# Optimization experiments

Hardware: AMD Instinct MI355X
Metric: run time of the kernel (lower is better)

The kernel has to match this reference:

```python
import jax, jax.numpy as jnp
import numpy as np

IN_DIM = 128
HID = 128
OUT = 128

def _linear(x, W, b):
    return x @ W + b

def setup_inputs() -> dict:
    key = jax.random.key(0)
    ks = jax.random.split(key, 16)
    B, N = 2, 512
    def w(k, fan_in, fan_out):
        lim = 1.0 / np.sqrt(fan_in)
        return jax.random.uniform(k, (fan_in, fan_out), jnp.float32, -lim, lim)
    def bvec(k, fan_in, fan_out):
        lim = 1.0 / np.sqrt(fan_in)
        return jax.random.uniform(k, (fan_out,), jnp.float32, -lim, lim)
    return {
        "features": jax.random.normal(ks[0], (B, N, IN_DIM), jnp.float32),
        "coords": jax.random.normal(ks[1], (B, N, 3), jnp.float32),
        "eW1": w(ks[2], 2 * IN_DIM + 1, HID), "eb1": bvec(ks[3], 2 * IN_DIM + 1, HID),
        "eW2": w(ks[4], HID, HID), "eb2": bvec(ks[5], HID, HID),
        "nW1": w(ks[6], IN_DIM + HID, HID), "nb1": bvec(ks[7], IN_DIM + HID, HID),
        "nW2": w(ks[8], HID, OUT), "nb2": bvec(ks[9], HID, OUT),
        "cW1": w(ks[10], HID, HID), "cb1": bvec(ks[11], HID, HID),
        "cW2": w(ks[12], HID, 1), "cb2": bvec(ks[13], HID, 1),
    }

def reference(features, coords, eW1, eb1, eW2, eb2, nW1, nb1, nW2, nb2, cW1, cb1, cW2, cb2):
    B, N, D = features.shape
    # pairwise coordinate differences and distances: (B, N, N, 3), (B, N, N, 1)
    coord_diff = coords[:, :, None, :] - coords[:, None, :, :]
    distances = jnp.sqrt(jnp.sum(coord_diff ** 2, axis=-1, keepdims=True) + 1e-8)
    # all-pairs edge features: (B, N, N, 2D+1)
    feat_i = jnp.broadcast_to(features[:, :, None, :], (B, N, N, D))
    feat_j = jnp.broadcast_to(features[:, None, :, :], (B, N, N, D))
    edge_features = jnp.concatenate([feat_i, feat_j, distances], axis=-1)
    edge_hidden = _linear(jax.nn.silu(_linear(edge_features, eW1, eb1)), eW2, eb2)
    # mean over neighbors j -> (B, N, HID)
    aggregated = jnp.mean(edge_hidden, axis=2)
    node_input = jnp.concatenate([features, aggregated], axis=-1)
    updated_features = _linear(jax.nn.silu(_linear(node_input, nW1, nb1)), nW2, nb2)
    # coordinate update
    coord_weights = _linear(jax.nn.silu(_linear(edge_hidden, cW1, cb1)), cW2, cb2)  # (B,N,N,1)
    updated_coords = coords + jnp.mean(coord_weights * coord_diff, axis=2)
    return (updated_features, updated_coords)
```

## Files before the change

kernel.cpp:

```cpp
#include <hip/hip_runtime.h>
#include <hip/hip_bf16.h>
#include <math.h>


typedef float f32x4 __attribute__((ext_vector_type(4)));
typedef short short8 __attribute__((ext_vector_type(8)));

#define MFMA16(a, b, c) __builtin_amdgcn_mfma_f32_16x16x32_bf16((a), (b), (c), 0, 0, 0)

__device__ __forceinline__ short f2bf(float x) {
    __hip_bfloat16 h = __float2bfloat16(x);
    union { __hip_bfloat16 h; short s; } v; v.h = h;
    return v.s;
}
__device__ __forceinline__ float bf2f(short s) {
    union { unsigned u; float f; } v; v.u = ((unsigned)(unsigned short)s) << 16;
    return v.f;
}
__device__ __forceinline__ float silu_f(float x) {
    return x * __builtin_amdgcn_rcpf(1.0f + __expf(-x));
}

__device__ __forceinline__ int swz(int row, int col) {
    int byte = (row << 8) | (col << 1);
    byte ^= (row & 7) << 4;
    return byte >> 1;
}

__global__ void egnn_pre(const float* __restrict__ feat, const float* __restrict__ eW1,
                         const float* __restrict__ eb1,
                         float* __restrict__ Abuf, float* __restrict__ Bbuf) {
    __shared__ float f[128];
    const int nid = blockIdx.x;
    const int t = threadIdx.x;
    if (t < 128) f[t] = feat[nid * 128 + t];
    __syncthreads();
    const int col  = t & 127;
    const int half = t >> 7;
    const float* W = eW1 + (size_t)half * 128 * 128 + col;
    float acc = half ? 0.f : eb1[col];
    #pragma unroll 8
    for (int k = 0; k < 128; ++k) acc += f[k] * W[(size_t)k * 128];
    if (half == 0) Abuf[nid * 128 + col] = acc;
    else           Bbuf[nid * 128 + col] = acc;
}

__global__ void egnn_wprep(const float* __restrict__ eW2, const float* __restrict__ cW1,
                           const float* __restrict__ eb2, const float* __restrict__ cb1,
                           unsigned short* __restrict__ MbfT, float* __restrict__ bias2ws) {
    const int a = blockIdx.x;
    const int c = threadIdx.x;
    if (a < 128) {
        float acc = 0.f;
        #pragma unroll 8
        for (int h = 0; h < 128; ++h) acc += eW2[a * 128 + h] * cW1[h * 128 + c];
        MbfT[c * 128 + a] = (unsigned short)f2bf(acc);
    } else {
        float acc = cb1[c];
        #pragma unroll 8
        for (int h = 0; h < 128; ++h) acc += eb2[h] * cW1[h * 128 + c];
        bias2ws[c] = acc;
    }
}

__global__ void __launch_bounds__(256, 2) egnn_main(
    const float* __restrict__ coords, const float* __restrict__ eW1,
    const float* __restrict__ cW2, const float* __restrict__ cb2,
    const float* __restrict__ Abuf, const float* __restrict__ Bbuf,
    const unsigned short* __restrict__ MbfT, const float* __restrict__ bias2ws,
    float* __restrict__ aggpart, float* __restrict__ coordpart)
{
    constexpr int Nn = 512;
    __shared__ __align__(16) short se[64 * 128];
    __shared__ float aw[128], wd[128];
    __shared__ float cdp[2][3][64];
    __shared__ float warr[2][4][64];
    __shared__ float aggred[16][128];
    __shared__ float cred[4][3];
    __shared__ float ci3[3];

    const int tid  = threadIdx.x;
    const int lane = tid & 63;
    const int wave = tid >> 6;
    const int bid  = blockIdx.x;
    const int node = bid >> 1;
    const int half = bid & 1;
    const int b    = node >> 9;

    if (tid < 128) {
        aw[tid] = Abuf[node * 128 + tid];
        wd[tid] = eW1[256 * 128 + tid];
    }
    if (tid == 0) {
        ci3[0] = coords[node * 3 + 0];
        ci3[1] = coords[node * 3 + 1];
        ci3[2] = coords[node * 3 + 2];
    }

    const int cfrag = wave * 32 + (lane & 15);
    const int koff  = (lane >> 4) * 8;
    short8 wfM[2][4];
    #pragma unroll
    for (int n2 = 0; n2 < 2; ++n2)
        #pragma unroll
        for (int k = 0; k < 4; ++k)
            wfM[n2][k] = *(const short8*)&MbfT[(size_t)(cfrag + n2 * 16) * 128 + k * 32 + koff];
    __syncthreads();

    const float b2_0  = bias2ws[cfrag], b2_1 = bias2ws[cfrag + 16];
    const float cw2_0 = cW2[cfrag],     cw2_1 = cW2[cfrag + 16];
    const float cb2v  = cb2[0];
    const float cix = ci3[0], ciy = ci3[1], ciz = ci3[2];

    const int jr = tid >> 2, cb = (tid & 3) * 32;
    const int rg = tid >> 4, c8 = (tid & 15) * 8;

    float ap[8];
    #pragma unroll
    for (int q = 0; q < 8; ++q) ap[q] = 0.f;
    float cax = 0.f, cay = 0.f, caz = 0.f;

    for (int t = 0; t < 4; ++t) {
        const int par = t & 1;
        {
            const int j = half * 256 + t * 64 + jr;
            const float dx = cix - coords[(b * Nn + j) * 3 + 0];
            const float dy = ciy - coords[(b * Nn + j) * 3 + 1];
            const float dz = ciz - coords[(b * Nn + j) * 3 + 2];
            const float dj = sqrtf(dx * dx + dy * dy + dz * dz + 1e-8f);
            if ((tid & 3) == 0) {
                cdp[par][0][jr] = dx; cdp[par][1][jr] = dy; cdp[par][2][jr] = dz;
            }
            const float* Bj = Bbuf + (size_t)(b * Nn + j) * 128 + cb;
            #pragma unroll
            for (int cc = 0; cc < 32; cc += 8) {
                f32x4 x0 = *(const f32x4*)(Bj + cc);
                f32x4 x1 = *(const f32x4*)(Bj + cc + 4);
                short8 v;
                #pragma unroll
                for (int r = 0; r < 4; ++r) {
                    const int c = cb + cc + r;
                    v[r] = f2bf(silu_f(aw[c] + x0[r] + dj * wd[c]));
                }
                #pragma unroll
                for (int r = 0; r < 4; ++r) {
                    const int c = cb + cc + 4 + r;
                    v[4 + r] = f2bf(silu_f(aw[c] + x1[r] + dj * wd[c]));
                }
                *(short8*)&se[swz(jr, cb + cc)] = v;
            }
        }
        __syncthreads();

        f32x4 acc[4][2];
        #pragma unroll
        for (int m = 0; m < 4; ++m) {
            acc[m][0] = (f32x4){b2_0, b2_0, b2_0, b2_0};
            acc[m][1] = (f32x4){b2_1, b2_1, b2_1, b2_1};
        }
        #pragma unroll
        for (int m = 0; m < 4; ++m)
            #pragma unroll
            for (int k = 0; k < 4; ++k) {
                short8 a = *(const short8*)&se[swz(m * 16 + (lane & 15), k * 32 + koff)];
                acc[m][0] = MFMA16(a, wfM[0][k], acc[m][0]);
                acc[m][1] = MFMA16(a, wfM[1][k], acc[m][1]);
            }

        #pragma unroll
        for (int r = 0; r < 4; ++r) {
            short8 v = *(const short8*)&se[swz(rg * 4 + r, c8)];
            #pragma unroll
            for (int q = 0; q < 8; ++q) ap[q] += bf2f(v[q]);
        }

        #pragma unroll
        for (int m = 0; m < 4; ++m)
            #pragma unroll
            for (int reg = 0; reg < 4; ++reg) {
                float v = silu_f(acc[m][0][reg]) * cw2_0
                        + silu_f(acc[m][1][reg]) * cw2_1;
                v += __shfl_xor(v, 1); v += __shfl_xor(v, 2);
                v += __shfl_xor(v, 4); v += __shfl_xor(v, 8);
                if ((lane & 15) == 0)
                    warr[par][wave][m * 16 + (lane >> 4) * 4 + reg] = v;
            }
        __syncthreads();

        if (lane < 16) {
            const int row = wave * 16 + lane;
            const float w = warr[par][0][row] + warr[par][1][row]
                          + warr[par][2][row] + warr[par][3][row] + cb2v;
            cax += w * cdp[par][0][row];
            cay += w * cdp[par][1][row];
            caz += w * cdp[par][2][row];
        }
    }

    #pragma unroll
    for (int q = 0; q < 8; ++q) aggred[rg][c8 + q] = ap[q];
    {
        float sx = cax, sy = cay, sz = caz;
        sx += __shfl_xor(sx, 1); sy += __shfl_xor(sy, 1); sz += __shfl_xor(sz, 1);
        sx += __shfl_xor(sx, 2); sy += __shfl_xor(sy, 2); sz += __shfl_xor(sz, 2);
        sx += __shfl_xor(sx, 4); sy += __shfl_xor(sy, 4); sz += __shfl_xor(sz, 4);
        sx += __shfl_xor(sx, 8); sy += __shfl_xor(sy, 8); sz += __shfl_xor(sz, 8);
        if (lane == 0) { cred[wave][0] = sx; cred[wave][1] = sy; cred[wave][2] = sz; }
    }
    __syncthreads();
    if (tid < 128) {
        float s = 0.f;
        #pragma unroll
        for (int g = 0; g < 16; ++g) s += aggred[g][tid];
        aggpart[(size_t)bid * 128 + tid] = s;
    }
    if (tid < 3) {
        coordpart[bid * 3 + tid] = cred[0][tid] + cred[1][tid] + cred[2][tid] + cred[3][tid];
    }
}

__global__ void egnn_post(
    const float* __restrict__ features, const float* __restrict__ coords,
    const float* __restrict__ eW2, const float* __restrict__ eb2,
    const float* __restrict__ nW1, const float* __restrict__ nb1,
    const float* __restrict__ nW2, const float* __restrict__ nb2,
    const float* __restrict__ aggpart, const float* __restrict__ coordpart,
    float* __restrict__ out_feat, float* __restrict__ out_coord)
{
    __shared__ float aggs[128], aggh[128], hbuf[128], fi[128];
    const int node = blockIdx.x;
    const int tid  = threadIdx.x;

    aggs[tid] = aggpart[(size_t)(node * 2) * 128 + tid]
              + aggpart[(size_t)(node * 2 + 1) * 128 + tid];
    fi[tid]   = features[node * 128 + tid];
    __syncthreads();
    {
        float acc = 0.f;
        #pragma unroll 4
        for (int c = 0; c < 128; ++c) acc += aggs[c] * eW2[c * 128 + tid];
        aggh[tid] = acc * (1.f / 512.f) + eb2[tid];
    }
    if (tid < 3) {
        out_coord[node * 3 + tid] = coords[node * 3 + tid]
            + (coordpart[(node * 2) * 3 + tid] + coordpart[(node * 2 + 1) * 3 + tid])
              * (1.f / 512.f);
    }
    __syncthreads();
    {
        float acc = nb1[tid];
        #pragma unroll 4
        for (int k = 0; k < 128; ++k) acc += fi[k] * nW1[k * 128 + tid];
        #pragma unroll 4
        for (int k = 0; k < 128; ++k) acc += aggh[k] * nW1[(128 + k) * 128 + tid];
        hbuf[tid] = silu_f(acc);
    }
    __syncthreads();
    {
        float acc = nb2[tid];
        #pragma unroll 4
        for (int k = 0; k < 128; ++k) acc += hbuf[k] * nW2[k * 128 + tid];
        out_feat[node * 128 + tid] = acc;
    }
}

extern "C" void kernel_launch(void* const* d_in, const int* in_sizes, int n_in,
                              void* d_out, int out_size, void* d_ws, size_t ws_size,
                              hipStream_t stream)
{
    const float* features = (const float*)d_in[0];
    const float* coords   = (const float*)d_in[1];
    const float* eW1 = (const float*)d_in[2];
    const float* eb1 = (const float*)d_in[3];
    const float* eW2 = (const float*)d_in[4];
    const float* eb2 = (const float*)d_in[5];
    const float* nW1 = (const float*)d_in[6];
    const float* nb1 = (const float*)d_in[7];
    const float* nW2 = (const float*)d_in[8];
    const float* nb2 = (const float*)d_in[9];
    const float* cW1 = (const float*)d_in[10];
    const float* cb1 = (const float*)d_in[11];
    const float* cW2 = (const float*)d_in[12];
    const float* cb2 = (const float*)d_in[13];

    float* out = (float*)d_out;
    float* out_feat  = out;
    float* out_coord = out + 2 * 512 * 128;

    float* Abuf      = (float*)d_ws;
    float* Bbuf      = Abuf + 2 * 512 * 128;
    unsigned short* MbfT = (unsigned short*)(Bbuf + 2 * 512 * 128);
    float* bias2ws   = (float*)(MbfT + 128 * 128);
    float* aggpart   = bias2ws + 128;
    float* coordpart = aggpart + 2048 * 128;

    egnn_pre<<<1024, 256, 0, stream>>>(features, eW1, eb1, Abuf, Bbuf);
    egnn_wprep<<<129, 128, 0, stream>>>(eW2, cW1, eb2, cb1, MbfT, bias2ws);
    egnn_main<<<2048, 256, 0, stream>>>(coords, eW1, cW2, cb2,
                                        Abuf, Bbuf, MbfT, bias2ws,
                                        aggpart, coordpart);
    egnn_post<<<1024, 128, 0, stream>>>(features, coords, eW2, eb2,
                                        nW1, nb1, nW2, nb2,
                                        aggpart, coordpart, out_feat, out_coord);
}
```

Measured before the change: 204.4 us.

## Split neighbours four ways with atomics, merge prep kernels, widen post kernel

Each node's neighbour range is now split across four blocks instead of two, and partial sums are combined with float atomicAdd into per-node buffers rather than written as separate partials. The two prep kernels are merged into one launch that also zeroes the accumulators. The post kernel uses 256 threads and splits each matvec across two thread groups. This aims to raise parallelism in the main kernel and cut one launch. In exchange it adds atomic traffic, doubles the per-block setup cost (weight fragment loads), and makes the floating-point summation order nondeterministic.

After: 184.9 us. -9.5%, faster.

```diff
diff --git a/kernel.cpp b/kernel.cpp
--- a/kernel.cpp
+++ b/kernel.cpp
@@ -27,39 +27,43 @@
     return byte >> 1;
 }
 
-__global__ void egnn_pre(const float* __restrict__ feat, const float* __restrict__ eW1,
-                         const float* __restrict__ eb1,
-                         float* __restrict__ Abuf, float* __restrict__ Bbuf) {
-    __shared__ float f[128];
-    const int nid = blockIdx.x;
+__global__ void egnn_prew(const float* __restrict__ feat, const float* __restrict__ eW1,
+                          const float* __restrict__ eb1,
+                          const float* __restrict__ eW2, const float* __restrict__ cW1,
+                          const float* __restrict__ eb2, const float* __restrict__ cb1,
+                          float* __restrict__ Abuf, float* __restrict__ Bbuf,
+                          unsigned short* __restrict__ MbfT, float* __restrict__ bias2ws,
+                          float* __restrict__ aggpart, float* __restrict__ coordpart) {
+    const int bid = blockIdx.x;
     const int t = threadIdx.x;
-    if (t < 128) f[t] = feat[nid * 128 + t];
-    __syncthreads();
-    const int col  = t & 127;
-    const int half = t >> 7;
-    const float* W = eW1 + (size_t)half * 128 * 128 + col;
-    float acc = half ? 0.f : eb1[col];
-    #pragma unroll 8
-    for (int k = 0; k < 128; ++k) acc += f[k] * W[(size_t)k * 128];
-    if (half == 0) Abuf[nid * 128 + col] = acc;
-    else           Bbuf[nid * 128 + col] = acc;
-}
-
-__global__ void egnn_wprep(const float* __restrict__ eW2, const float* __restrict__ cW1,
-                           const float* __restrict__ eb2, const float* __restrict__ cb1,
-                           unsigned short* __restrict__ MbfT, float* __restrict__ bias2ws) {
-    const int a = blockIdx.x;
-    const int c = threadIdx.x;
-    if (a < 128) {
-        float acc = 0.f;
+    if (bid < 1024) {
+        __shared__ float f[128];
+        if (t < 128) f[t] = feat[bid * 128 + t];
+        __syncthreads();
+        const int col  = t & 127;
+        const int half = t >> 7;
+        const float* W = eW1 + (size_t)half * 128 * 128 + col;
+        float acc = half ? 0.f : eb1[col];
         #pragma unroll 8
-        for (int h = 0; h < 128; ++h) acc += eW2[a * 128 + h] * cW1[h * 128 + c];
-        MbfT[c * 128 + a] = (unsigned short)f2bf(acc);
+        for (int k = 0; k < 128; ++k) acc += f[k] * W[(size_t)k * 128];
+        if (half == 0) Abuf[bid * 128 + col] = acc;
+        else           Bbuf[bid * 128 + col] = acc;
+        if (t < 128) aggpart[(size_t)bid * 128 + t] = 0.f;
+        if (t < 3)   coordpart[bid * 3 + t] = 0.f;
     } else {
-        float acc = cb1[c];
-        #pragma unroll 8
-        for (int h = 0; h < 128; ++h) acc += eb2[h] * cW1[h * 128 + c];
-        bias2ws[c] = acc;
+        const int idx = (bid - 1024) * 2 + (t >> 7);
+        const int c = t & 127;
+        if (idx < 128) {
+            float acc = 0.f;
+            #pragma unroll 8
+            for (int h = 0; h < 128; ++h) acc += eW2[idx * 128 + h] * cW1[h * 128 + c];
+            MbfT[c * 128 + idx] = (unsigned short)f2bf(acc);
+        } else if (idx == 128) {
+            float acc = cb1[c];
+            #pragma unroll 8
+            for (int h = 0; h < 128; ++h) acc += eb2[h] * cW1[h * 128 + c];
+            bias2ws[c] = acc;
+        }
     }
 }
 
@@ -83,8 +87,8 @@
     const int lane = tid & 63;
     const int wave = tid >> 6;
     const int bid  = blockIdx.x;
-    const int node = bid >> 1;
-    const int half = bid & 1;
+    const int node = bid >> 2;
+    const int quad = bid & 3;
     const int b    = node >> 9;
 
     if (tid < 128) {
@@ -120,10 +124,10 @@
     for (int q = 0; q < 8; ++q) ap[q] = 0.f;
     float cax = 0.f, cay = 0.f, caz = 0.f;
 
-    for (int t = 0; t < 4; ++t) {
+    for (int t = 0; t < 2; ++t) {
         const int par = t & 1;
         {
-            const int j = half * 256 + t * 64 + jr;
+            const int j = quad * 128 + t * 64 + jr;
             const float dx = cix - coords[(b * Nn + j) * 3 + 0];
             const float dy = ciy - coords[(b * Nn + j) * 3 + 1];
             const float dz = ciz - coords[(b * Nn + j) * 3 + 2];
@@ -212,10 +216,11 @@
         float s = 0.f;
         #pragma unroll
         for (int g = 0; g < 16; ++g) s += aggred[g][tid];
-        aggpart[(size_t)bid * 128 + tid] = s;
+        atomicAdd(&aggpart[(size_t)node * 128 + tid], s);
     }
     if (tid < 3) {
-        coordpart[bid * 3 + tid] = cred[0][tid] + cred[1][tid] + cred[2][tid] + cred[3][tid];
+        atomicAdd(&coordpart[node * 3 + tid],
+                  cred[0][tid] + cred[1][tid] + cred[2][tid] + cred[3][tid]);
     }
 }
 
@@ -227,40 +232,46 @@
     const float* __restrict__ aggpart, const float* __restrict__ coordpart,
     float* __restrict__ out_feat, float* __restrict__ out_coord)
 {
-    __shared__ float aggs[128], aggh[128], hbuf[128], fi[128];
+    __shared__ float aggs[128], aggh[128], hbuf[128], fi[128], part[128];
     const int node = blockIdx.x;
     const int tid  = threadIdx.x;
-
-    aggs[tid] = aggpart[(size_t)(node * 2) * 128 + tid]
-              + aggpart[(size_t)(node * 2 + 1) * 128 + tid];
-    fi[tid]   = features[node * 128 + tid];
+    const int c = tid & 127, g = tid >> 7;
+
+    if (tid < 128) {
+        aggs[tid] = aggpart[(size_t)node * 128 + tid];
+        fi[tid]   = features[node * 128 + tid];
+    }
+    if (tid < 3)
+        out_coord[node * 3 + tid] = coords[node * 3 + tid]
+                                  + coordpart[node * 3 + tid] * (1.f / 512.f);
     __syncthreads();
     {
         float acc = 0.f;
-        #pragma unroll 4
-        for (int c = 0; c < 128; ++c) acc += aggs[c] * eW2[c * 128 + tid];
-        aggh[tid] = acc * (1.f / 512.f) + eb2[tid];
-    }
-    if (tid < 3) {
-        out_coord[node * 3 + tid] = coords[node * 3 + tid]
-            + (coordpart[(node * 2) * 3 + tid] + coordpart[(node * 2 + 1) * 3 + tid])
-              * (1.f / 512.f);
-    }
-    __syncthreads();
+        #pragma unroll 8
+        for (int k = g * 64; k < g * 64 + 64; ++k) acc += aggs[k] * eW2[k * 128 + c];
+        if (g == 1) part[c] = acc;
+        __syncthreads();
+        if (g == 0) aggh[c] = (acc + part[c]) * (1.f / 512.f) + eb2[c];
+        __syncthreads();
+    }
     {
-        float acc = nb1[tid];
-        #pragma unroll 4
-        for (int k = 0; k < 128; ++k) acc += fi[k] * nW1[k * 128 + tid];
-        #pragma unroll 4
-        for (int k = 0; k < 128; ++k) acc += aggh[k] * nW1[(128 + k) * 128 + tid];
-        hbuf[tid] = silu_f(acc);
-    }
-    __syncthreads();
+        float acc = (g == 0) ? nb1[c] : 0.f;
+        const float* src = (g == 0) ? fi : aggh;
+        const float* W = nW1 + (size_t)(g << 7) * 128 + c;
+        #pragma unroll 8
+        for (int k = 0; k < 128; ++k) acc += src[k] * W[(size_t)k * 128];
+        if (g == 1) part[c] = acc;
+        __syncthreads();
+        if (g == 0) hbuf[c] = silu_f(acc + part[c]);
+        __syncthreads();
+    }
     {
-        float acc = nb2[tid];
-        #pragma unroll 4
-        for (int k = 0; k < 128; ++k) acc += hbuf[k] * nW2[k * 128 + tid];
-        out_feat[node * 128 + tid] = acc;
+        float acc = (g == 0) ? nb2[c] : 0.f;
+        #pragma unroll 8
+        for (int k = g * 64; k < g * 64 + 64; ++k) acc += hbuf[k] * nW2[k * 128 + c];
+        if (g == 1) part[c] = acc;
+        __syncthreads();
+        if (g == 0) out_feat[node * 128 + c] = acc + part[c];
     }
 }
 
@@ -292,14 +303,14 @@
     unsigned short* MbfT = (unsigned short*)(Bbuf + 2 * 512 * 128);
     float* bias2ws   = (float*)(MbfT + 128 * 128);
     float* aggpart   = bias2ws + 128;
-    float* coordpart = aggpart + 2048 * 128;
-
-    egnn_pre<<<1024, 256, 0, stream>>>(features, eW1, eb1, Abuf, Bbuf);
-    egnn_wprep<<<129, 128, 0, stream>>>(eW2, cW1, eb2, cb1, MbfT, bias2ws);
-    egnn_main<<<2048, 256, 0, stream>>>(coords, eW1, cW2, cb2,
+    float* coordpart = aggpart + 1024 * 128;
+
+    egnn_prew<<<1089, 256, 0, stream>>>(features, eW1, eb1, eW2, cW1, eb2, cb1,
+                                        Abuf, Bbuf, MbfT, bias2ws, aggpart, coordpart);
+    egnn_main<<<4096, 256, 0, stream>>>(coords, eW1, cW2, cb2,
                                         Abuf, Bbuf, MbfT, bias2ws,
                                         aggpart, coordpart);
-    egnn_post<<<1024, 128, 0, stream>>>(features, coords, eW2, eb2,
+    egnn_post<<<1024, 256, 0, stream>>>(features, coords, eW2, eb2,
                                         nW1, nb1, nW2, nb2,
                                         aggpart, coordpart, out_feat, out_coord);
 }
```
